# Kernel optimization log

Hardware: AMD Instinct MI355X
Metric: run time of the kernel (lower is better)

## Reference

```python
import jax, jax.numpy as jnp
import numpy as np

B, C, H, W, MODES, RANK = 16, 128, 128, 128, 16, 8


def setup_inputs() -> dict:
    key = jax.random.key(0)
    ks = jax.random.split(key, 8)
    scale = 1.0 / (C * C)
    lr_scale = 0.02
    return {
        "x": jax.random.normal(ks[0], (B, C, H, W), dtype=jnp.float32),
        "w_real": scale * jax.random.normal(ks[1], (C, C, MODES, MODES), dtype=jnp.float32),
        "w_imag": scale * jax.random.normal(ks[2], (C, C, MODES, MODES), dtype=jnp.float32),
        "u_real": lr_scale * jax.random.normal(ks[3], (C, RANK, MODES, MODES), dtype=jnp.float32),
        "u_imag": lr_scale * jax.random.normal(ks[4], (C, RANK, MODES, MODES), dtype=jnp.float32),
        "v_real": lr_scale * jax.random.normal(ks[5], (C, RANK, MODES, MODES), dtype=jnp.float32),
        "v_imag": lr_scale * jax.random.normal(ks[6], (C, RANK, MODES, MODES), dtype=jnp.float32),
        "skip_w": (1.0 / np.sqrt(C)) * jax.random.normal(ks[7], (C, C), dtype=jnp.float32),
    }


def physical_act(x):
    # f(x) = x * exp(-|x|^2)
    return x * jnp.exp(-jnp.abs(x) ** 2)


def reference(x, w_real, w_imag, u_real, u_imag, v_real, v_imag, skip_w):
    Bb, Cc, Hh, Ww = x.shape
    # 1x1 conv skip path == channel matmul
    x_skip = jnp.einsum('oc,bchw->bohw', skip_w, x)
    # FFT to spectral domain: (B, C, H, W//2+1) complex64
    x_ft = jnp.fft.rfft2(x, norm='ortho')
    W_ft = x_ft.shape[-1]
    m1 = min(w_real.shape[-2], Hh)
    m2 = min(w_real.shape[-1], W_ft)
    # truncated-mode complex diagonal operator D (per-frequency channel mix)
    D = (w_real + 1j * w_imag)[:, :, :m1, :m2]          # (O, I, m1, m2)
    x_top = x_ft[:, :, :m1, :m2]                         # (B, I, m1, m2)
    out_top = jnp.einsum('bimn,oimn->bomn', x_top, D)
    # low-rank cross-frequency mixer UV*
    U = (u_real + 1j * u_imag)[:, :, :m1, :m2]           # (O, R, m1, m2)
    V = (v_real + 1j * v_imag)[:, :, :m1, :m2]           # (I, R, m1, m2)
    z = jnp.einsum('bimn,irmn->br', x_top, jnp.conj(V))  # (B, R)
    out_top = out_top + jnp.einsum('ormn,br->bomn', U, z)
    # scatter back into zero-padded full spectrum
    out_ft = jnp.zeros(x_ft.shape, dtype=x_ft.dtype).at[:, :, :m1, :m2].set(out_top)
    x_spectral = jnp.fft.irfft2(out_ft, s=(Hh, Ww), norm='ortho')
    out = x_spectral + x_skip
    return physical_act(out)
```

## Files before the change

### kernel.cpp

```cpp
#include <hip/hip_runtime.h>
#include <math.h>

#define TAB_OFF 0
#define XTOP_OFF 16384
#define Z_OFF (16384 + 1048576)
#define OTOP_OFF (Z_OFF + 256)
#define TF_OFF (OTOP_OFF + 1048576)
#define T2F_OFF (TF_OFF + 4096)
#define SWF_OFF (T2F_OFF + 2048)

using bf16x8 = __attribute__((ext_vector_type(8))) short;
using s16x4  = __attribute__((ext_vector_type(4))) short;
using f32x16 = __attribute__((ext_vector_type(16))) float;

__device__ inline unsigned short bf_rnd(float v) {
  return (unsigned short)((__float_as_uint(v) + 0x8000u) >> 16);
}
__device__ inline void bf_split(float v, unsigned short& hi, unsigned short& lo) {
  unsigned u = __float_as_uint(v);
  hi = (unsigned short)(u >> 16);
  float r = v - __uint_as_float(u & 0xFFFF0000u);
  lo = (unsigned short)(__float_as_uint(r) >> 16);
}
__device__ inline bf16x8 ldfrag(const unsigned short* p) {
  s16x4 a = *(const s16x4*)p;
  s16x4 b = *(const s16x4*)(p + 4);
  bf16x8 r;
  r[0] = a[0]; r[1] = a[1]; r[2] = a[2]; r[3] = a[3];
  r[4] = b[0]; r[5] = b[1]; r[6] = b[2]; r[7] = b[3];
  return r;
}
__device__ inline bf16x8 ldfrag_sw(const unsigned short* base, int row, int koff) {
  int byte = row * 256 + ((koff * 2) ^ ((row & 7) << 4));
  return ldfrag((const unsigned short*)((const char*)base + byte));
}

__global__ __launch_bounds__(256) void k_prep(const float* __restrict__ sw,
                                              float* __restrict__ tab,
                                              unsigned short* __restrict__ tf,
                                              unsigned short* __restrict__ t2f,
                                              unsigned short* __restrict__ swf,
                                              float4* __restrict__ zdst) {
  int idx = blockIdx.x * 256 + threadIdx.x;
  for (int i = idx; i < 262208; i += 40960)
    zdst[i] = make_float4(0.f, 0.f, 0.f, 0.f);

  if (idx < 16384) {
    int which = idx >> 11, rem = idx & 2047;
    int a, j;
    if (which == 4 || which == 5) { a = rem & 127; j = rem >> 7; }
    else { a = rem >> 4; j = rem & 15; }
    int p = (a * j) & 127;
    float ang = (float)p * (float)(3.14159265358979323846 / 64.0);
    float cv = cosf(ang), sv = sinf(ang);
    float v;
    switch (which) {
      case 0: v = cv * (1.f / 128.f); break;
      case 1: v = -sv * (1.f / 128.f); break;
      case 2: v = cv; break;
      case 3: v = sv; break;
      case 4: v = cv; break;
      case 5: v = sv; break;
      case 6: v = ((rem & 15) == 0 ? 1.f : 2.f) * cv * (1.f / 128.f); break;
      default: v = ((rem & 15) == 0 ? 1.f : 2.f) * (-sv) * (1.f / 128.f); break;
    }
    tab[idx] = v;
  } else if (idx < 20480) {
    int r = idx - 16384;
    int np = r >> 7, k = r & 127;
    int n = np & 15;
    int p = (k * n) & 127;
    float ang = (float)p * (float)(3.14159265358979323846 / 64.0);
    float v = (np < 16 ? cosf(ang) : -sinf(ang)) * (1.f / 128.f);
    unsigned short hi, lo;
    bf_split(v, hi, lo);
    tf[np * 128 + k] = hi;
    tf[4096 + np * 128 + k] = lo;
  } else if (idx < 24576) {
    int r = idx - 20480;
    int w = r >> 5, np = r & 31;
    int n = np & 15;
    int p = (w * n) & 127;
    float ang = (float)p * (float)(3.14159265358979323846 / 64.0);
    float cn = (n == 0) ? 1.f : 2.f;
    float v = (np < 16 ? cosf(ang) : -sinf(ang)) * cn * (1.f / 128.f);
    t2f[r] = bf_rnd(v);
  } else if (idx < 40960) {
    int r = idx - 24576;
    int o = r >> 7, k = r & 127;
    unsigned short hb, lb;
    bf_split(sw[o * 128 + k], hb, lb);
    int kc = k >> 5, ks = (k >> 4) & 1, kh = (k >> 3) & 1, j = k & 7;
    int f0 = (kc * 2 + ks) * 2;
    swf[(f0 + 0) * 2048 + o * 16 + kh * 8 + j] = hb;
    swf[(f0 + 1) * 2048 + o * 16 + kh * 8 + j] = lb;
  }
}

__global__ __launch_bounds__(256) void k_fwd(const float* __restrict__ x,
                                             const unsigned short* __restrict__ tf,
                                             const float* __restrict__ tab,
                                             const float* __restrict__ vre,
                                             const float* __restrict__ vim,
                                             float* __restrict__ xtop,
                                             float* __restrict__ zout) {
  __shared__ unsigned short Xh[128 * 128];
  __shared__ unsigned short Tfh[32 * 128];
  __shared__ unsigned short Tfl[32 * 128];
  __shared__ float red[4][16];
  const int cd = blockIdx.x;
  const int c = ((cd & 7) << 4) | (cd >> 3);
  const int b = blockIdx.y;
  const int t = threadIdx.x;
  const int lane = t & 63, wv = t >> 6;

  #pragma unroll
  for (int it = 0; it < 32; ++it) {
    int idx = it * 256 + t;
    int part = idx >> 12, rem = idx & 4095;
    int row = rem >> 7, k = rem & 127;
    unsigned short v = tf[part * 4096 + rem];
    unsigned short* dst = part ? Tfl : Tfh;
    *(unsigned short*)((char*)dst + row * 256 + ((k * 2) ^ ((row & 7) << 4))) = v;
  }
  const float* img = x + (((size_t)(b * 128 + c)) << 14);
  #pragma unroll
  for (int it = 0; it < 16; ++it) {
    int flat = it * 256 + t;
    int h = flat >> 5, wq = flat & 31;
    float4 v = *(const float4*)(img + (size_t)flat * 4);
    s16x4 pk;
    pk[0] = (short)bf_rnd(v.x); pk[1] = (short)bf_rnd(v.y);
    pk[2] = (short)bf_rnd(v.z); pk[3] = (short)bf_rnd(v.w);
    *(s16x4*)((char*)Xh + h * 256 + ((wq * 8) ^ ((h & 7) << 4))) = pk;
  }
  __syncthreads();

  f32x16 acc;
  #pragma unroll
  for (int e = 0; e < 16; ++e) acc[e] = 0.f;
  const int orow = wv * 32 + (lane & 31);
  const int bcol = lane & 31;
  const int kh8 = (lane >> 5) * 8;
  #pragma unroll
  for (int kc8 = 0; kc8 < 8; ++kc8) {
    int kfull = kc8 * 16 + kh8;
    bf16x8 a  = ldfrag_sw(Xh, orow, kfull);
    bf16x8 th = ldfrag_sw(Tfh, bcol, kfull);
    bf16x8 tl = ldfrag_sw(Tfl, bcol, kfull);
    acc = __builtin_amdgcn_mfma_f32_32x32x16_bf16(a, th, acc, 0, 0, 0);
    acc = __builtin_amdgcn_mfma_f32_32x32x16_bf16(a, tl, acc, 0, 0, 0);
  }
  __syncthreads();

  float* Arp = (float*)Xh;
  float* Aip = Arp + 16 * 132;
  {
    const int col = lane & 31;
    #pragma unroll
    for (int r = 0; r < 16; ++r) {
      int h = wv * 32 + (r & 3) + 8 * (r >> 2) + 4 * (lane >> 5);
      if (col < 16) Arp[col * 132 + h] = acc[r];
      else          Aip[(col - 16) * 132 + h] = acc[r];
    }
  }
  __syncthreads();

  float xr = 0.f, xi = 0.f;
  {
    const int m = t >> 4, n = t & 15;
    const float* tc = tab + 8192 + m * 128;
    const float* ts = tab + 10240 + m * 128;
    const float* ar = Arp + n * 132;
    const float* ai = Aip + n * 132;
    #pragma unroll 8
    for (int h4 = 0; h4 < 128; h4 += 4) {
      float4 av = *(const float4*)(ar + h4);
      float4 iv = *(const float4*)(ai + h4);
      float4 cv = *(const float4*)(tc + h4);
      float4 sv = *(const float4*)(ts + h4);
      xr += av.x * cv.x + iv.x * sv.x;  xi += iv.x * cv.x - av.x * sv.x;
      xr += av.y * cv.y + iv.y * sv.y;  xi += iv.y * cv.y - av.y * sv.y;
      xr += av.z * cv.z + iv.z * sv.z;  xi += iv.z * cv.z - av.z * sv.z;
      xr += av.w * cv.w + iv.w * sv.w;  xi += iv.w * cv.w - av.w * sv.w;
    }
    size_t base = ((size_t)(b * 128 + c)) * 512 + (size_t)t * 2;
    xtop[base] = xr; xtop[base + 1] = xi;
  }

  {
    float zr[8], zi[8];
    #pragma unroll
    for (int r = 0; r < 8; ++r) {
      float vr = vre[(size_t)(c * 8 + r) * 256 + t];
      float vi = vim[(size_t)(c * 8 + r) * 256 + t];
      zr[r] = xr * vr + xi * vi;
      zi[r] = xi * vr - xr * vi;
    }
    #pragma unroll
    for (int r = 0; r < 8; ++r)
      for (int off = 32; off > 0; off >>= 1) {
        zr[r] += __shfl_down(zr[r], off);
        zi[r] += __shfl_down(zi[r], off);
      }
    if (lane == 0) {
      #pragma unroll
      for (int r = 0; r < 8; ++r) { red[wv][r * 2] = zr[r]; red[wv][r * 2 + 1] = zi[r]; }
    }
    __syncthreads();
    if (t < 16) atomicAdd(&zout[b * 16 + t], red[0][t] + red[1][t] + red[2][t] + red[3][t]);
  }
}

__global__ __launch_bounds__(256) void k_mix(const float* __restrict__ xtop,
                                             const float* __restrict__ wre,
                                             const float* __restrict__ wim,
                                             const float* __restrict__ ure,
                                             const float* __restrict__ uim,
                                             const float* __restrict__ z,
                                             float* __restrict__ otop) {
  int o0 = blockIdx.x * 4, b0 = blockIdx.y * 2, ic = blockIdx.z, t = threadIdx.x;
  float ar[2][4], ai[2][4];
  #pragma unroll
  for (int bb = 0; bb < 2; ++bb)
    #pragma unroll
    for (int oo = 0; oo < 4; ++oo) { ar[bb][oo] = 0.f; ai[bb][oo] = 0.f; }
  const float* x0 = xtop + ((size_t)(b0 * 128)) * 512;
  const float* x1 = x0 + 128 * 512;
  for (int i = ic * 16; i < ic * 16 + 16; ++i) {
    float x0r = x0[i * 512 + t * 2], x0i = x0[i * 512 + t * 2 + 1];
    float x1r = x1[i * 512 + t * 2], x1i = x1[i * 512 + t * 2 + 1];
    #pragma unroll
    for (int oo = 0; oo < 4; ++oo) {
      size_t di = (size_t)((o0 + oo) * 128 + i) * 256 + t;
      float dr = wre[di], dj = wim[di];
      ar[0][oo] += dr * x0r - dj * x0i; ai[0][oo] += dr * x0i + dj * x0r;
      ar[1][oo] += dr * x1r - dj * x1i; ai[1][oo] += dr * x1i + dj * x1r;
    }
  }
  if (ic == 0) {
    float zr[2][8], zi[2][8];
    #pragma unroll
    for (int bb = 0; bb < 2; ++bb)
      #pragma unroll
      for (int r = 0; r < 8; ++r) {
        zr[bb][r] = z[(b0 + bb) * 16 + r * 2];
        zi[bb][r] = z[(b0 + bb) * 16 + r * 2 + 1];
      }
    #pragma unroll
    for (int oo = 0; oo < 4; ++oo)
      #pragma unroll
      for (int r = 0; r < 8; ++r) {
        float urv = ure[(size_t)((o0 + oo) * 8 + r) * 256 + t];
        float uiv = uim[(size_t)((o0 + oo) * 8 + r) * 256 + t];
        #pragma unroll
        for (int bb = 0; bb < 2; ++bb) {
          ar[bb][oo] += urv * zr[bb][r] - uiv * zi[bb][r];
          ai[bb][oo] += urv * zi[bb][r] + uiv * zr[bb][r];
        }
      }
  }
  #pragma unroll
  for (int bb = 0; bb < 2; ++bb)
    #pragma unroll
    for (int oo = 0; oo < 4; ++oo) {
      size_t oi = ((size_t)((b0 + bb) * 128 + o0 + oo) * 256 + (size_t)t) * 2;
      atomicAdd(&otop[oi], ar[bb][oo]);
      atomicAdd(&otop[oi + 1], ai[bb][oo]);
    }
}

__global__ __launch_bounds__(256) void k_out(const float* __restrict__ x,
                                             const unsigned short* __restrict__ swf,
                                             const unsigned short* __restrict__ t2f,
                                             const float* __restrict__ otop,
                                             const float* __restrict__ tab,
                                             float* __restrict__ out) {
  __shared__ unsigned short Ylds[128 * 36];
  __shared__ unsigned short Bh[128 * 36], Bl[128 * 36];
  const int hd = blockIdx.x;
  const int h = ((hd & 7) << 4) | (hd >> 3);
  const int b = blockIdx.y;
  const int t = threadIdx.x;
  const int lane = t & 63, wv = t >> 6;
  const int kh8 = (lane >> 5) * 8;
  const int col = lane & 31;
  const int o_lane = wv * 32 + col;

  {
    int o = t >> 1, nh = (t & 1) * 8;
    float yr[8], yi[8];
    #pragma unroll
    for (int j = 0; j < 8; ++j) { yr[j] = 0.f; yi[j] = 0.f; }
    const float* xb = otop + ((size_t)(b * 128 + o)) * 512 + nh * 2;
    #pragma unroll 4
    for (int m = 0; m < 16; ++m) {
      float cm = tab[4096 + h * 16 + m];
      float sm = tab[6144 + h * 16 + m];
      float4 q0 = *(const float4*)(xb + m * 32 + 0);
      float4 q1 = *(const float4*)(xb + m * 32 + 4);
      float4 q2 = *(const float4*)(xb + m * 32 + 8);
      float4 q3 = *(const float4*)(xb + m * 32 + 12);
      yr[0] += q0.x * cm - q0.y * sm; yi[0] += q0.x * sm + q0.y * cm;
      yr[1] += q0.z * cm - q0.w * sm; yi[1] += q0.z * sm + q0.w * cm;
      yr[2] += q1.x * cm - q1.y * sm; yi[2] += q1.x * sm + q1.y * cm;
      yr[3] += q1.z * cm - q1.w * sm; yi[3] += q1.z * sm + q1.w * cm;
      yr[4] += q2.x * cm - q2.y * sm; yi[4] += q2.x * sm + q2.y * cm;
      yr[5] += q2.z * cm - q2.w * sm; yi[5] += q2.z * sm + q2.w * cm;
      yr[6] += q3.x * cm - q3.y * sm; yi[6] += q3.x * sm + q3.y * cm;
      yr[7] += q3.z * cm - q3.w * sm; yi[7] += q3.z * sm + q3.w * cm;
    }
    #pragma unroll
    for (int j = 0; j < 8; ++j) {
      Ylds[o * 36 + nh + j] = bf_rnd(yr[j]);
      Ylds[o * 36 + 16 + nh + j] = bf_rnd(yi[j]);
    }
  }

  f32x16 acc[4];
  #pragma unroll
  for (int nt = 0; nt < 4; ++nt)
    #pragma unroll
    for (int e = 0; e < 16; ++e) acc[nt][e] = 0.f;

  const int cofs = t >> 7;
  const int wB = t & 127;
  const float* xbase = x + (size_t)b * 2097152 + (size_t)h * 128 + wB;

  #pragma unroll
  for (int kc = 0; kc < 4; ++kc) {
    float xv[16];
    #pragma unroll
    for (int it = 0; it < 16; ++it)
      xv[it] = xbase[(size_t)(kc * 32 + it * 2 + cofs) * 16384];
    bf16x8 ah[2], al[2];
    #pragma unroll
    for (int ks = 0; ks < 2; ++ks) {
      const unsigned short* base = swf + (size_t)((kc * 2 + ks) * 2) * 2048 + o_lane * 16 + kh8;
      ah[ks] = *(const bf16x8*)base;
      al[ks] = *(const bf16x8*)(base + 2048);
    }
    __syncthreads();
    #pragma unroll
    for (int it = 0; it < 16; ++it) {
      int cl = it * 2 + cofs;
      unsigned short hb, lb;
      bf_split(xv[it], hb, lb);
      Bh[wB * 36 + cl] = hb; Bl[wB * 36 + cl] = lb;
    }
    __syncthreads();
    #pragma unroll
    for (int ks = 0; ks < 2; ++ks) {
      const int kb = ks * 16 + kh8;
      #pragma unroll
      for (int nt = 0; nt < 4; ++nt) {
        bf16x8 bh_ = ldfrag(&Bh[(nt * 32 + col) * 36 + kb]);
        bf16x8 bl_ = ldfrag(&Bl[(nt * 32 + col) * 36 + kb]);
        acc[nt] = __builtin_amdgcn_mfma_f32_32x32x16_bf16(ah[ks], bh_, acc[nt], 0, 0, 0);
        acc[nt] = __builtin_amdgcn_mfma_f32_32x32x16_bf16(ah[ks], bl_, acc[nt], 0, 0, 0);
        acc[nt] = __builtin_amdgcn_mfma_f32_32x32x16_bf16(al[ks], bh_, acc[nt], 0, 0, 0);
      }
    }
  }

  #pragma unroll
  for (int ks = 0; ks < 2; ++ks) {
    const int kb = ks * 16 + kh8;
    bf16x8 ya = ldfrag(&Ylds[o_lane * 36 + kb]);
    #pragma unroll
    for (int nt = 0; nt < 4; ++nt) {
      bf16x8 tb = *(const bf16x8*)(t2f + (nt * 32 + col) * 32 + kb);
      acc[nt] = __builtin_amdgcn_mfma_f32_32x32x16_bf16(ya, tb, acc[nt], 0, 0, 0);
    }
  }

  #pragma unroll
  for (int nt = 0; nt < 4; ++nt) {
    int w = nt * 32 + col;
    #pragma unroll
    for (int r = 0; r < 16; ++r) {
      int o = wv * 32 + (r & 3) + 8 * (r >> 2) + 4 * (lane >> 5);
      float v = acc[nt][r];
      out[((size_t)(b * 128 + o)) * 16384 + (size_t)h * 128 + w] = v * __expf(-v * v);
    }
  }
}

extern "C" void kernel_launch(void* const* d_in, const int* in_sizes, int n_in,
                              void* d_out, int out_size, void* d_ws, size_t ws_size,
                              hipStream_t stream) {
  const float* x  = (const float*)d_in[0];
  const float* wr = (const float*)d_in[1];
  const float* wi = (const float*)d_in[2];
  const float* ur = (const float*)d_in[3];
  const float* ui = (const float*)d_in[4];
  const float* vr = (const float*)d_in[5];
  const float* vi = (const float*)d_in[6];
  const float* sw = (const float*)d_in[7];
  float* out  = (float*)d_out;
  float* ws   = (float*)d_ws;
  float* tab  = ws + TAB_OFF;
  float* xtop = ws + XTOP_OFF;
  float* z    = ws + Z_OFF;
  float* otop = ws + OTOP_OFF;
  unsigned short* tf  = (unsigned short*)(ws + TF_OFF);
  unsigned short* t2f = (unsigned short*)(ws + T2F_OFF);
  unsigned short* swf = (unsigned short*)(ws + SWF_OFF);

  hipLaunchKernelGGL(k_prep, dim3(160), dim3(256), 0, stream, sw, tab, tf, t2f, swf,
                     (float4*)z);
  hipLaunchKernelGGL(k_fwd,  dim3(128, 16), dim3(256), 0, stream, x, tf, tab, vr, vi, xtop, z);
  hipLaunchKernelGGL(k_mix,  dim3(32, 8, 8), dim3(256), 0, stream, xtop, wr, wi, ur, ui, z, otop);
  hipLaunchKernelGGL(k_out,  dim3(128, 16), dim3(256), 0, stream, x, swf, t2f, otop, tab, out);
}
```

Before: 181.2 us.

## Restructure spectral mix to avoid atomics and drop otop zeroing

The channel-mixing kernel is remapped so each block owns one mode row, 16 output channels and 8 batches. The input-channel reduction is split across two half-blocks and combined through shared memory, and results are written with plain vector stores instead of atomics. Because otop is now fully overwritten, the prep kernel only zeroes the small z accumulator instead of the whole 1 MB otop buffer. Loads become float4 vectorized. The trade-off is a much smaller grid (256 blocks of 512 threads), which lowers parallelism, and each thread loops over 64 input channels serially.

```diff
diff --git a/kernel.cpp b/kernel.cpp
--- a/kernel.cpp
+++ b/kernel.cpp
@@ -42,8 +42,7 @@
                                               unsigned short* __restrict__ swf,
                                               float4* __restrict__ zdst) {
   int idx = blockIdx.x * 256 + threadIdx.x;
-  for (int i = idx; i < 262208; i += 40960)
-    zdst[i] = make_float4(0.f, 0.f, 0.f, 0.f);
+  if (idx < 64) zdst[idx] = make_float4(0.f, 0.f, 0.f, 0.f);
 
   if (idx < 16384) {
     int which = idx >> 11, rem = idx & 2047;
@@ -212,62 +211,84 @@
   }
 }
 
-__global__ __launch_bounds__(256) void k_mix(const float* __restrict__ xtop,
+__global__ __launch_bounds__(512) void k_mix(const float* __restrict__ xtop,
                                              const float* __restrict__ wre,
                                              const float* __restrict__ wim,
                                              const float* __restrict__ ure,
                                              const float* __restrict__ uim,
                                              const float* __restrict__ z,
                                              float* __restrict__ otop) {
-  int o0 = blockIdx.x * 4, b0 = blockIdx.y * 2, ic = blockIdx.z, t = threadIdx.x;
-  float ar[2][4], ai[2][4];
-  #pragma unroll
-  for (int bb = 0; bb < 2; ++bb)
-    #pragma unroll
-    for (int oo = 0; oo < 4; ++oo) { ar[bb][oo] = 0.f; ai[bb][oo] = 0.f; }
-  const float* x0 = xtop + ((size_t)(b0 * 128)) * 512;
-  const float* x1 = x0 + 128 * 512;
-  for (int i = ic * 16; i < ic * 16 + 16; ++i) {
-    float x0r = x0[i * 512 + t * 2], x0i = x0[i * 512 + t * 2 + 1];
-    float x1r = x1[i * 512 + t * 2], x1i = x1[i * 512 + t * 2 + 1];
-    #pragma unroll
-    for (int oo = 0; oo < 4; ++oo) {
-      size_t di = (size_t)((o0 + oo) * 128 + i) * 256 + t;
-      float dr = wre[di], dj = wim[di];
-      ar[0][oo] += dr * x0r - dj * x0i; ai[0][oo] += dr * x0i + dj * x0r;
-      ar[1][oo] += dr * x1r - dj * x1i; ai[1][oo] += dr * x1i + dj * x1r;
-    }
-  }
-  if (ic == 0) {
-    float zr[2][8], zi[2][8];
-    #pragma unroll
-    for (int bb = 0; bb < 2; ++bb)
-      #pragma unroll
-      for (int r = 0; r < 8; ++r) {
-        zr[bb][r] = z[(b0 + bb) * 16 + r * 2];
-        zi[bb][r] = z[(b0 + bb) * 16 + r * 2 + 1];
-      }
-    #pragma unroll
-    for (int oo = 0; oo < 4; ++oo)
-      #pragma unroll
-      for (int r = 0; r < 8; ++r) {
-        float urv = ure[(size_t)((o0 + oo) * 8 + r) * 256 + t];
-        float uiv = uim[(size_t)((o0 + oo) * 8 + r) * 256 + t];
-        #pragma unroll
-        for (int bb = 0; bb < 2; ++bb) {
-          ar[bb][oo] += urv * zr[bb][r] - uiv * zi[bb][r];
-          ai[bb][oo] += urv * zi[bb][r] + uiv * zr[bb][r];
-        }
-      }
-  }
-  #pragma unroll
-  for (int bb = 0; bb < 2; ++bb)
-    #pragma unroll
-    for (int oo = 0; oo < 4; ++oo) {
-      size_t oi = ((size_t)((b0 + bb) * 128 + o0 + oo) * 256 + (size_t)t) * 2;
-      atomicAdd(&otop[oi], ar[bb][oo]);
-      atomicAdd(&otop[oi + 1], ai[bb][oo]);
-    }
+  __shared__ float partial[256 * 17];
+  const int m = blockIdx.x, og = blockIdx.y, bg = blockIdx.z;
+  const int t = threadIdx.x;
+  const int ol = t & 15;
+  const int bl = (t >> 4) & 7;
+  const int nh = ((t >> 7) & 1) * 8;
+  const int ih = t >> 8;
+  const int o = og * 16 + ol;
+  const int b = bg * 8 + bl;
+
+  float ar[8], ai[8];
+  #pragma unroll
+  for (int j = 0; j < 8; ++j) { ar[j] = 0.f; ai[j] = 0.f; }
+
+  const float* xb  = xtop + (size_t)(b * 128) * 512 + (m * 16 + nh) * 2;
+  const float* wrb = wre  + (size_t)(o * 128) * 256 + m * 16 + nh;
+  const float* wib = wim  + (size_t)(o * 128) * 256 + m * 16 + nh;
+  #pragma unroll 4
+  for (int i = ih * 64; i < ih * 64 + 64; ++i) {
+    float4 x0 = *(const float4*)(xb + (size_t)i * 512 + 0);
+    float4 x1 = *(const float4*)(xb + (size_t)i * 512 + 4);
+    float4 x2 = *(const float4*)(xb + (size_t)i * 512 + 8);
+    float4 x3 = *(const float4*)(xb + (size_t)i * 512 + 12);
+    float4 w0 = *(const float4*)(wrb + (size_t)i * 256);
+    float4 w1 = *(const float4*)(wrb + (size_t)i * 256 + 4);
+    float4 v0 = *(const float4*)(wib + (size_t)i * 256);
+    float4 v1 = *(const float4*)(wib + (size_t)i * 256 + 4);
+    ar[0] += w0.x * x0.x - v0.x * x0.y;  ai[0] += w0.x * x0.y + v0.x * x0.x;
+    ar[1] += w0.y * x0.z - v0.y * x0.w;  ai[1] += w0.y * x0.w + v0.y * x0.z;
+    ar[2] += w0.z * x1.x - v0.z * x1.y;  ai[2] += w0.z * x1.y + v0.z * x1.x;
+    ar[3] += w0.w * x1.z - v0.w * x1.w;  ai[3] += w0.w * x1.w + v0.w * x1.z;
+    ar[4] += w1.x * x2.x - v1.x * x2.y;  ai[4] += w1.x * x2.y + v1.x * x2.x;
+    ar[5] += w1.y * x2.z - v1.y * x2.w;  ai[5] += w1.y * x2.w + v1.y * x2.z;
+    ar[6] += w1.z * x3.x - v1.z * x3.y;  ai[6] += w1.z * x3.y + v1.z * x3.x;
+    ar[7] += w1.w * x3.z - v1.w * x3.w;  ai[7] += w1.w * x3.w + v1.w * x3.z;
+  }
+
+  if (ih == 1) {
+    float* p = partial + (t - 256) * 17;
+    #pragma unroll
+    for (int j = 0; j < 8; ++j) { p[j * 2] = ar[j]; p[j * 2 + 1] = ai[j]; }
+  }
+  __syncthreads();
+  if (ih == 0) {
+    const float* p = partial + t * 17;
+    #pragma unroll
+    for (int j = 0; j < 8; ++j) { ar[j] += p[j * 2]; ai[j] += p[j * 2 + 1]; }
+    #pragma unroll
+    for (int r = 0; r < 8; ++r) {
+      float zr = z[b * 16 + r * 2], zi_ = z[b * 16 + r * 2 + 1];
+      const float* ub = ure + (size_t)(o * 8 + r) * 256 + m * 16 + nh;
+      const float* vb = uim + (size_t)(o * 8 + r) * 256 + m * 16 + nh;
+      float4 u0 = *(const float4*)ub, u1 = *(const float4*)(ub + 4);
+      float4 q0 = *(const float4*)vb, q1 = *(const float4*)(vb + 4);
+      ar[0] += u0.x * zr - q0.x * zi_;  ai[0] += u0.x * zi_ + q0.x * zr;
+      ar[1] += u0.y * zr - q0.y * zi_;  ai[1] += u0.y * zi_ + q0.y * zr;
+      ar[2] += u0.z * zr - q0.z * zi_;  ai[2] += u0.z * zi_ + q0.z * zr;
+      ar[3] += u0.w * zr - q0.w * zi_;  ai[3] += u0.w * zi_ + q0.w * zr;
+      ar[4] += u1.x * zr - q1.x * zi_;  ai[4] += u1.x * zi_ + q1.x * zr;
+      ar[5] += u1.y * zr - q1.y * zi_;  ai[5] += u1.y * zi_ + q1.y * zr;
+      ar[6] += u1.z * zr - q1.z * zi_;  ai[6] += u1.z * zi_ + q1.z * zr;
+      ar[7] += u1.w * zr - q1.w * zi_;  ai[7] += u1.w * zi_ + q1.w * zr;
+    }
+    float* dst = otop + (size_t)(b * 128 + o) * 512 + (m * 16 + nh) * 2;
+    #pragma unroll
+    for (int j = 0; j < 4; ++j) {
+      float4 s;
+      s.x = ar[j * 2]; s.y = ai[j * 2]; s.z = ar[j * 2 + 1]; s.w = ai[j * 2 + 1];
+      *(float4*)(dst + j * 4) = s;
+    }
+  }
 }
 
 __global__ __launch_bounds__(256) void k_out(const float* __restrict__ x,
@@ -410,6 +431,6 @@
   hipLaunchKernelGGL(k_prep, dim3(160), dim3(256), 0, stream, sw, tab, tf, t2f, swf,
                      (float4*)z);
   hipLaunchKernelGGL(k_fwd,  dim3(128, 16), dim3(256), 0, stream, x, tf, tab, vr, vi, xtop, z);
-  hipLaunchKernelGGL(k_mix,  dim3(32, 8, 8), dim3(256), 0, stream, xtop, wr, wi, ur, ui, z, otop);
+  hipLaunchKernelGGL(k_mix,  dim3(16, 8, 2), dim3(512), 0, stream, xtop, wr, wi, ur, ui, z, otop);
   hipLaunchKernelGGL(k_out,  dim3(128, 16), dim3(256), 0, stream, x, swf, t2f, otop, tab, out);
 }
```

New measurement: 207.7 us. 14.6% more time.
